# Kernel optimization log

Hardware: AMD Instinct MI355X
Metric: run time of the kernel (lower is better)

The kernel has to match this reference:

```python
import jax, jax.numpy as jnp
import numpy as np

B, S, D = 2, 2048, 1024
H = 16
HD = D // H
WINDOW = 128
SCALE = HD ** -0.5


def setup_inputs() -> dict:
    key = jax.random.key(0)
    ks = jax.random.split(key, 5)
    x = jax.random.normal(ks[0], (B, S, D), dtype=jnp.float32)
    # nn.Linear(dim, 3*dim) and nn.Linear(dim, dim), stored as [in, out] for x @ W
    w_qkv = jax.random.normal(ks[1], (D, 3 * D), dtype=jnp.float32) * (D ** -0.5)
    b_qkv = jax.random.normal(ks[2], (3 * D,), dtype=jnp.float32) * 0.02
    w_out = jax.random.normal(ks[3], (D, D), dtype=jnp.float32) * (D ** -0.5)
    b_out = jax.random.normal(ks[4], (D,), dtype=jnp.float32) * 0.02
    return {"x": x, "w_qkv": w_qkv, "b_qkv": b_qkv, "w_out": w_out, "b_out": b_out}


def _local_mask(seq_len):
    idx = jnp.arange(seq_len)
    band = jnp.abs(idx[:, None] - idx[None, :]) <= WINDOW // 2
    return jnp.where(band, 0.0, -jnp.inf).astype(jnp.float32)  # [S, S]


def reference(x, w_qkv, b_qkv, w_out, b_out):
    b, s, _ = x.shape
    qkv = x @ w_qkv + b_qkv                       # [B, S, 3D]
    qkv = qkv.reshape(b, s, 3, H, HD).transpose(2, 0, 3, 1, 4)  # [3, B, H, S, HD]
    q, k, v = qkv[0], qkv[1], qkv[2]
    mask = _local_mask(s)                          # [S, S]
    scores = jnp.einsum("bhqd,bhkd->bhqk", q, k) * SCALE + mask
    attn = jax.nn.softmax(scores, axis=-1)         # dropout is identity at eval
    out = jnp.einsum("bhqk,bhkd->bhqd", attn, v)   # [B, H, S, HD]
    out = out.transpose(0, 2, 1, 3).reshape(b, s, D)
    return out @ w_out + b_out
```

## Files before the change

### kernel.cpp

```cpp
#include <hip/hip_runtime.h>
#include <hip/hip_bf16.h>

typedef short bf16x8 __attribute__((ext_vector_type(8)));
typedef float f32x4 __attribute__((ext_vector_type(4)));
typedef unsigned short ushort_t;

#define SQ 2048
#define DIM 1024
#define NH 16
#define HD 64

__device__ __forceinline__ ushort_t f2bf(float f) {
    __hip_bfloat16 h = __float2bfloat16(f);
    return *reinterpret_cast<ushort_t*>(&h);
}

__device__ __forceinline__ void load_lds16(const void* g, void* l) {
    __builtin_amdgcn_global_load_lds(
        (const __attribute__((address_space(1))) unsigned int*)g,
        (__attribute__((address_space(3))) unsigned int*)l, 16, 0, 0);
}

__global__ void prep_kernel(const float* __restrict__ x, ushort_t* __restrict__ xb,
                            const float* __restrict__ w_qkv, ushort_t* __restrict__ wqkvT,
                            const float* __restrict__ w_out, ushort_t* __restrict__ woutT) {
    __shared__ ushort_t tile[32][33];
    const int bid = blockIdx.x;
    const int tid = threadIdx.x;
    if (bid < 1024) {
        int i = bid * 256 + tid;
        const int stride = 1024 * 256;
        const int n4 = 4096 * 1024 / 4;
        for (; i < n4; i += stride) {
            float4 f = reinterpret_cast<const float4*>(x)[i];
            ushort4 o;
            o.x = f2bf(f.x); o.y = f2bf(f.y); o.z = f2bf(f.z); o.w = f2bf(f.w);
            reinterpret_cast<ushort4*>(xb)[i] = o;
        }
        return;
    }
    const float* in; ushort_t* out; int R, C, idx;
    if (bid < 4096) { idx = bid - 1024; in = w_qkv; out = wqkvT; R = 1024; C = 3072;
        int cx = idx % 96, ry = idx / 96;
        int c0 = cx * 32, r0 = ry * 32;
        int tx = tid & 31, ty = tid >> 5;
#pragma unroll
        for (int i = 0; i < 32; i += 8)
            tile[ty + i][tx] = f2bf(in[(size_t)(r0 + ty + i) * C + c0 + tx]);
        __syncthreads();
#pragma unroll
        for (int i = 0; i < 32; i += 8)
            out[(size_t)(c0 + ty + i) * R + r0 + tx] = tile[tx][ty + i];
        return;
    }
    idx = bid - 4096; in = w_out; out = woutT; R = 1024; C = 1024;
    int cx = idx % 32, ry = idx / 32;
    int c0 = cx * 32, r0 = ry * 32;
    int tx = tid & 31, ty = tid >> 5;
#pragma unroll
    for (int i = 0; i < 32; i += 8)
        tile[ty + i][tx] = f2bf(in[(size_t)(r0 + ty + i) * C + c0 + tx]);
    __syncthreads();
#pragma unroll
    for (int i = 0; i < 32; i += 8)
        out[(size_t)(c0 + ty + i) * R + r0 + tx] = tile[tx][ty + i];
}

__global__ void transpose_v(const ushort_t* __restrict__ qkv, ushort_t* __restrict__ vt) {
    __shared__ ushort_t tile[32][33];
    int s0 = blockIdx.x * 32, d0 = blockIdx.y * 32;
    int bh = blockIdx.z;
    int b = bh >> 4, h = bh & 15;
    const ushort_t* src = qkv + (size_t)(b * SQ) * 3072 + 2048 + h * 64;
    ushort_t* dst = vt + (size_t)bh * HD * SQ;
    int tx = threadIdx.x, ty = threadIdx.y;
#pragma unroll
    for (int i = 0; i < 32; i += 8)
        tile[ty + i][tx] = src[(size_t)(s0 + ty + i) * 3072 + d0 + tx];
    __syncthreads();
#pragma unroll
    for (int i = 0; i < 32; i += 8)
        dst[(size_t)(d0 + ty + i) * SQ + s0 + tx] = tile[tx][ty + i];
}


#define STAGE_U(Gptr, ldk, grow0, kcol, regionbase)                          \
  { int row_ = tid >> 3;                                                      \
    int sc_ = (tid & 7) ^ (row_ & 7);                                         \
    load_lds16((Gptr) + (size_t)((grow0) + row_) * (ldk) + (kcol) + sc_ * 8,  \
               (regionbase) + tid * 16); }

#define DS_A192(BASE, EXTRA)                                                  \
  _Pragma("unroll") for (int kk_ = 0; kk_ < 2; ++kk_)                         \
  _Pragma("unroll") for (int m_ = 0; m_ < 4; ++m_)                            \
    a[kk_][m_] = *reinterpret_cast<const bf16x8*>((BASE) + (EXTRA) + offA[kk_][m_]);

#define DS_B192(BASE)                                                         \
  _Pragma("unroll") for (int kk_ = 0; kk_ < 2; ++kk_)                         \
  _Pragma("unroll") for (int n_ = 0; n_ < 3; ++n_)                            \
    b[kk_][n_] = *reinterpret_cast<const bf16x8*>((BASE) + offB[kk_][n_]);

#define BAR_LGKM                                                              \
  __builtin_amdgcn_s_barrier();                                               \
  asm volatile("s_waitcnt lgkmcnt(0)" ::: "memory");                          \
  __builtin_amdgcn_sched_barrier(0);

#define MFMA_Q(MQ)                                                            \
  __builtin_amdgcn_s_setprio(1);                                              \
  _Pragma("unroll") for (int kk_ = 0; kk_ < 2; ++kk_)                         \
  _Pragma("unroll") for (int m_ = 0; m_ < 4; ++m_)                            \
  _Pragma("unroll") for (int n_ = 0; n_ < 3; ++n_)                            \
    acc[(MQ)*4 + m_][n_] = __builtin_amdgcn_mfma_f32_16x16x32_bf16(           \
        a[kk_][m_], b[kk_][n_], acc[(MQ)*4 + m_][n_], 0, 0, 0);               \
  __builtin_amdgcn_s_setprio(0);

__global__ __launch_bounds__(512, 2)
void gemm192_bt(const ushort_t* __restrict__ A, const ushort_t* __restrict__ Bt,
                const float* __restrict__ bias, ushort_t* __restrict__ Cout,
                int M, int N, int K, int nbn) {
    __shared__ char sm[114688];
    const int tid = threadIdx.x;
    const int lane = tid & 63;
    const int w = tid >> 6;
    const int wm = w >> 2, wn = w & 3;
    const int r = lane & 15, hi = lane >> 4;

    const int cpx = gridDim.x >> 3;
    const int bid = blockIdx.x;
    const int x = (bid & 7) * cpx + (bid >> 3);
    const int bm = x / nbn, bn = x % nbn;
    const int m0 = bm * 256, n0 = bn * 192;

    const int NT = K >> 6;
    const int NI = NT >> 1;

    char* const A0 = sm;
    char* const B0 = sm + 32768;
    char* const A1 = sm + 57344;
    char* const B1 = sm + 90112;

    int offA[2][4], offB[2][3];
#pragma unroll
    for (int kk = 0; kk < 2; ++kk) {
#pragma unroll
        for (int m = 0; m < 4; ++m) {
            int rowL = wm * 128 + m * 16 + r;
            offA[kk][m] = rowL * 128 + (((kk * 4 + hi) ^ (rowL & 7)) * 16);
        }
#pragma unroll
        for (int n = 0; n < 3; ++n) {
            int rowL = wn * 48 + n * 16 + r;
            offB[kk][n] = rowL * 128 + (((kk * 4 + hi) ^ (rowL & 7)) * 16);
        }
    }

    f32x4 acc[8][3];
#pragma unroll
    for (int am = 0; am < 8; ++am)
#pragma unroll
        for (int an = 0; an < 3; ++an) acc[am][an] = (f32x4){0.f, 0.f, 0.f, 0.f};

    bf16x8 a[2][4], b[2][3];

    STAGE_U(A,  K, m0,        0, A0);
    STAGE_U(A,  K, m0 + 64,   0, A0 + 8192);
    STAGE_U(A,  K, m0 + 128,  0, A0 + 16384);
    STAGE_U(A,  K, m0 + 192,  0, A0 + 24576);
    STAGE_U(Bt, K, n0,        0, B0);
    STAGE_U(Bt, K, n0 + 64,   0, B0 + 8192);
    STAGE_U(Bt, K, n0 + 128,  0, B0 + 16384);
    STAGE_U(A,  K, m0,       64, A1);
    STAGE_U(A,  K, m0 + 128, 64, A1 + 16384);
    asm volatile("s_waitcnt vmcnt(2)" ::: "memory");
    __builtin_amdgcn_s_barrier();

    for (int i = 0; i < NI; ++i) {
        const int k1 = (2 * i + 1) * 64;
        const int k2 = ((2 * i + 2) % NT) * 64;
        const int k3 = ((2 * i + 3) % NT) * 64;

        STAGE_U(A,  K, m0 + 64,  k1, A1 + 8192);
        STAGE_U(A,  K, m0 + 192, k1, A1 + 24576);
        STAGE_U(Bt, K, n0,       k1, B1);
        STAGE_U(Bt, K, n0 + 64,  k1, B1 + 8192);
        STAGE_U(Bt, K, n0 + 128, k1, B1 + 16384);
        DS_A192(A0, 0); DS_B192(B0);
        BAR_LGKM; MFMA_Q(0);
        __builtin_amdgcn_s_barrier();

        STAGE_U(A, K, m0,       k2, A0);
        STAGE_U(A, K, m0 + 128, k2, A0 + 16384);
        DS_A192(A0, 8192);
        BAR_LGKM; MFMA_Q(1);
        asm volatile("s_waitcnt vmcnt(2)" ::: "memory");
        __builtin_amdgcn_s_barrier();

        STAGE_U(A,  K, m0 + 64,  k2, A0 + 8192);
        STAGE_U(A,  K, m0 + 192, k2, A0 + 24576);
        STAGE_U(Bt, K, n0,       k2, B0);
        STAGE_U(Bt, K, n0 + 64,  k2, B0 + 8192);
        STAGE_U(Bt, K, n0 + 128, k2, B0 + 16384);
        DS_A192(A1, 0); DS_B192(B1);
        BAR_LGKM; MFMA_Q(0);
        __builtin_amdgcn_s_barrier();

        STAGE_U(A, K, m0,       k3, A1);
        STAGE_U(A, K, m0 + 128, k3, A1 + 16384);
        DS_A192(A1, 8192);
        BAR_LGKM; MFMA_Q(1);
        asm volatile("s_waitcnt vmcnt(2)" ::: "memory");
        __builtin_amdgcn_s_barrier();
    }

#pragma unroll
    for (int am = 0; am < 8; ++am) {
        int rowg = m0 + wm * 128 + (am >> 2) * 64 + (am & 3) * 16 + hi * 4;
#pragma unroll
        for (int an = 0; an < 3; ++an) {
            int colg = n0 + wn * 48 + an * 16 + r;
            float bv = bias[colg];
#pragma unroll
            for (int j = 0; j < 4; ++j) {
                float v = acc[am][an][j] + bv;
                Cout[(size_t)(rowg + j) * N + colg] = f2bf(v);
            }
        }
    }
}

__global__ __launch_bounds__(256)
void gemm_bt2(const ushort_t* __restrict__ A, const ushort_t* __restrict__ Bt,
              const float* __restrict__ bias, float* __restrict__ Cout,
              int M, int N, int K) {
    __shared__ char sA[16384];
    __shared__ char sB[8192];
    const int tid = threadIdx.x;
    const int m0 = blockIdx.y * 128, n0 = blockIdx.x * 64;
    const int w = tid >> 6, lane = tid & 63;
    const int wr = w >> 1, wc = w & 1;
    const int r = lane & 15, hi = lane >> 4;

    f32x4 acc[4][2];
#pragma unroll
    for (int m = 0; m < 4; ++m)
#pragma unroll
        for (int n = 0; n < 2; ++n) acc[m][n] = (f32x4){0.f, 0.f, 0.f, 0.f};

    for (int k0 = 0; k0 < K; k0 += 64) {
#pragma unroll
        for (int i = 0; i < 4; ++i) {
            int task = i * 256 + tid;
            int row = task >> 3;
            int sc = (task & 7) ^ (row & 7);
            load_lds16(A + (size_t)(m0 + row) * K + k0 + sc * 8, sA + task * 16);
        }
#pragma unroll
        for (int i = 0; i < 2; ++i) {
            int task = i * 256 + tid;
            int row = task >> 3;
            int sc = (task & 7) ^ (row & 7);
            load_lds16(Bt + (size_t)(n0 + row) * K + k0 + sc * 8, sB + task * 16);
        }
        __syncthreads();

#pragma unroll
        for (int ks = 0; ks < 2; ++ks) {
            bf16x8 af[4], bfr[2];
#pragma unroll
            for (int m = 0; m < 4; ++m) {
                int row = wr * 64 + m * 16 + r;
                af[m] = *reinterpret_cast<const bf16x8*>(
                    sA + row * 128 + (((ks * 4 + hi) ^ (row & 7)) * 16));
            }
#pragma unroll
            for (int n = 0; n < 2; ++n) {
                int row = wc * 32 + n * 16 + r;
                bfr[n] = *reinterpret_cast<const bf16x8*>(
                    sB + row * 128 + (((ks * 4 + hi) ^ (row & 7)) * 16));
            }
#pragma unroll
            for (int m = 0; m < 4; ++m)
#pragma unroll
                for (int n = 0; n < 2; ++n)
                    acc[m][n] = __builtin_amdgcn_mfma_f32_16x16x32_bf16(
                        af[m], bfr[n], acc[m][n], 0, 0, 0);
        }
        __syncthreads();
    }

#pragma unroll
    for (int n = 0; n < 2; ++n) {
        int colg = n0 + wc * 32 + n * 16 + r;
        float bv = bias[colg];
#pragma unroll
        for (int m = 0; m < 4; ++m) {
            int rowg = m0 + wr * 64 + m * 16 + hi * 4;
#pragma unroll
            for (int j = 0; j < 4; ++j)
                Cout[(size_t)(rowg + j) * N + colg] = acc[m][n][j] + bv;
        }
    }
}

__global__ __launch_bounds__(256, 4)
void attn_kernel(const ushort_t* __restrict__ qkv, const ushort_t* __restrict__ vt,
                 ushort_t* __restrict__ attn_out) {
    __shared__ uint4 smem4[50176 / 16];
    char* smem = (char*)smem4;

    const int bid0 = blockIdx.x;
    const int bid = (bid0 & 7) * 128 + (bid0 >> 3);
    const int qb = bid & 31;
    const int h = (bid >> 5) & 15;
    const int b = bid >> 9;
    const int q0 = qb * 64;
    const int kstart = (q0 - 64 > 0) ? (q0 - 64) : 0;

    const int tid = threadIdx.x;
    const int lane = tid & 63;
    const int w = tid >> 6;
    const int r = lane & 15, hi = lane >> 4;

#pragma unroll
    for (int i = 0; i < 6; ++i) {
        int task = i * 256 + tid;
        int row = task >> 3, ch = task & 7;
        int key = kstart + row;
        uint4 v = make_uint4(0u, 0u, 0u, 0u);
        if (key < SQ)
            v = *reinterpret_cast<const uint4*>(
                qkv + (size_t)(b * SQ + key) * 3072 + 1024 + h * 64 + ch * 8);
        int byte = row * 128 + ch * 16; byte ^= (row & 7) << 4;
        *reinterpret_cast<uint4*>(smem + byte) = v;
    }
    {
        const ushort_t* vtb = vt + (size_t)(b * NH + h) * HD * SQ;
        int d = tid >> 2, cp = tid & 3;
#pragma unroll
        for (int i = 0; i < 6; ++i) {
            int c = cp + i * 4;
            uint4 v = make_uint4(0u, 0u, 0u, 0u);
            int k8 = kstart + c * 8;
            if (k8 < SQ)
                v = *reinterpret_cast<const uint4*>(vtb + (size_t)d * SQ + k8);
            int byte = d * 384 + (((c & 7) ^ (d & 7)) * 16) + ((c >> 3) * 128);
            *reinterpret_cast<uint4*>(smem + 25600 + byte) = v;
        }
    }

    const ushort_t* qrow = qkv + (size_t)(b * SQ + q0 + w * 16 + r) * 3072 + h * 64;
    bf16x8 aq0 = *reinterpret_cast<const bf16x8*>(qrow + hi * 8);
    bf16x8 aq1 = *reinterpret_cast<const bf16x8*>(qrow + 32 + hi * 8);

    __syncthreads();

    const int delta = q0 - kstart;
    const int base = w * 16 + delta;
    int tmin = (base - 64) >> 4; if (tmin < 0) tmin = 0;
    int tmax = (base + 79) >> 4;
    int tcap = (SQ - 1 - kstart) >> 4; if (tmax > tcap) tmax = tcap;
    if (tmax > 11) tmax = 11;
    const int ksmin = tmin >> 1, ksmax = tmax >> 1;

    f32x4 acc[12];
#pragma unroll
    for (int t = 0; t < 12; ++t) acc[t] = (f32x4){0.f, 0.f, 0.f, 0.f};
#pragma unroll
    for (int t = 0; t < 12; ++t) {
        if (t < tmin || t > tmax) continue;
#pragma unroll
        for (int ks = 0; ks < 2; ++ks) {
            int row = t * 16 + r;
            int byte = row * 128 + ks * 64 + hi * 16; byte ^= (row & 7) << 4;
            bf16x8 bk = *reinterpret_cast<const bf16x8*>(smem + byte);
            acc[t] = __builtin_amdgcn_mfma_f32_16x16x32_bf16(
                ks == 0 ? aq0 : aq1, bk, acc[t], 0, 0, 0);
        }
    }

    float mrow[4], lrow[4];
#pragma unroll
    for (int t = 0; t < 12; ++t) {
        if (t < tmin || t > tmax) continue;
        int key = kstart + t * 16 + r;
#pragma unroll
        for (int j = 0; j < 4; ++j) {
            int qrow_g = q0 + w * 16 + hi * 4 + j;
            int dd = key - qrow_g; if (dd < 0) dd = -dd;
            bool valid = (key < SQ) && (dd <= 64);
            acc[t][j] = valid ? acc[t][j] * 0.125f : -1e30f;
        }
    }
#pragma unroll
    for (int j = 0; j < 4; ++j) {
        float m = -1e30f;
#pragma unroll
        for (int t = 0; t < 12; ++t) {
            if (t < tmin || t > tmax) continue;
            m = fmaxf(m, acc[t][j]);
        }
        m = fmaxf(m, __shfl_xor(m, 1));
        m = fmaxf(m, __shfl_xor(m, 2));
        m = fmaxf(m, __shfl_xor(m, 4));
        m = fmaxf(m, __shfl_xor(m, 8));
        mrow[j] = m;
    }
#pragma unroll
    for (int j = 0; j < 4; ++j) {
        float s = 0.f;
#pragma unroll
        for (int t = 0; t < 12; ++t) {
            if (t < tmin || t > tmax) continue;
            float p = __expf(acc[t][j] - mrow[j]);
            acc[t][j] = p;
            s += p;
        }
        s += __shfl_xor(s, 1);
        s += __shfl_xor(s, 2);
        s += __shfl_xor(s, 4);
        s += __shfl_xor(s, 8);
        lrow[j] = s;
    }

    __syncthreads();

#pragma unroll
    for (int t = 0; t < 12; ++t) {
        int col = t * 16 + r;
        bool inb = (t >= tmin) && (t <= tmax);
#pragma unroll
        for (int j = 0; j < 4; ++j) {
            int rowL = w * 16 + hi * 4 + j;
            ushort_t pv = inb ? f2bf(acc[t][j]) : (ushort_t)0;
            *reinterpret_cast<ushort_t*>(smem + rowL * 400 + col * 2) = pv;
        }
    }

    f32x4 oacc[4];
#pragma unroll
    for (int dt = 0; dt < 4; ++dt) oacc[dt] = (f32x4){0.f, 0.f, 0.f, 0.f};
#pragma unroll
    for (int ks = 0; ks < 6; ++ks) {
        if (ks < ksmin || ks > ksmax) continue;
        int k0 = ks * 32 + hi * 8;
        bf16x8 ap = *reinterpret_cast<const bf16x8*>(
            smem + (w * 16 + r) * 400 + k0 * 2);
        int cch = ks * 4 + hi;
#pragma unroll
        for (int dt = 0; dt < 4; ++dt) {
            int d = dt * 16 + r;
            int byte = d * 384 + (((cch & 7) ^ (d & 7)) * 16) + ((cch >> 3) * 128);
            bf16x8 bv = *reinterpret_cast<const bf16x8*>(smem + 25600 + byte);
            oacc[dt] = __builtin_amdgcn_mfma_f32_16x16x32_bf16(ap, bv, oacc[dt], 0, 0, 0);
        }
    }

    float inv[4];
#pragma unroll
    for (int j = 0; j < 4; ++j) inv[j] = 1.0f / lrow[j];
#pragma unroll
    for (int dt = 0; dt < 4; ++dt) {
        int d = dt * 16 + r;
#pragma unroll
        for (int j = 0; j < 4; ++j) {
            int q = q0 + w * 16 + hi * 4 + j;
            attn_out[(size_t)(b * SQ + q) * 1024 + h * 64 + d] = f2bf(oacc[dt][j] * inv[j]);
        }
    }
}

extern "C" void kernel_launch(void* const* d_in, const int* in_sizes, int n_in,
                              void* d_out, int out_size, void* d_ws, size_t ws_size,
                              hipStream_t stream) {
    const float* x     = (const float*)d_in[0];
    const float* w_qkv = (const float*)d_in[1];
    const float* b_qkv = (const float*)d_in[2];
    const float* w_out = (const float*)d_in[3];
    const float* b_out = (const float*)d_in[4];
    float* out = (float*)d_out;

    char* ws = (char*)d_ws;
    ushort_t* xb    = (ushort_t*)(ws);
    ushort_t* wqkvT = (ushort_t*)(ws + 8388608);
    ushort_t* woutT = (ushort_t*)(ws + 14680064);
    ushort_t* qkv   = (ushort_t*)(ws + 16777216);
    ushort_t* aout  = (ushort_t*)(ws + 41943040);
    ushort_t* vtbuf = (ushort_t*)(ws + 50331648);

    prep_kernel<<<5120, 256, 0, stream>>>(x, xb, w_qkv, wqkvT, w_out, woutT);

    gemm192_bt<<<256, 512, 0, stream>>>(xb, wqkvT, b_qkv, qkv, 4096, 3072, 1024, 16);
    transpose_v<<<dim3(64, 2, 32), dim3(32, 8), 0, stream>>>(qkv, vtbuf);
    attn_kernel<<<1024, 256, 0, stream>>>(qkv, vtbuf, aout);
    gemm_bt2<<<dim3(16, 32), 256, 0, stream>>>(aout, woutT, b_out, out, 4096, 1024, 1024);
}
```

Before: 81.88 us.

## Replace output projection GEMM with double-buffered 128x128 four-phase pipelined kernel

The output projection GEMM, previously a 128x64 tile kernel that loads and then computes in single-buffered steps with two barriers per k-step, is replaced by a 512-thread 128x128 tile kernel. It double-buffers A and B in LDS and staggers global-to-LDS loads across four phases so loads overlap MFMA work, and it raises MFMA priority with s_setprio. Block IDs are swizzled across 8 groups. It reuses the STAGE_U and BAR_LGKM macros from the QKV GEMM. Grid size drops from 512 to 256 blocks, which may reduce occupancy on a 256-CU part.

```diff
diff --git a/kernel.cpp b/kernel.cpp
--- a/kernel.cpp
+++ b/kernel.cpp
@@ -228,76 +228,125 @@
     }
 }
 
-__global__ __launch_bounds__(256)
-void gemm_bt2(const ushort_t* __restrict__ A, const ushort_t* __restrict__ Bt,
-              const float* __restrict__ bias, float* __restrict__ Cout,
-              int M, int N, int K) {
-    __shared__ char sA[16384];
-    __shared__ char sB[8192];
+
+#define G2_DSA(BASE, MQ)                                                      \
+  _Pragma("unroll") for (int kk_ = 0; kk_ < 2; ++kk_)                         \
+  _Pragma("unroll") for (int m_ = 0; m_ < 2; ++m_)                            \
+    a2[kk_][m_] = *reinterpret_cast<const bf16x8*>((BASE) + offA2[kk_][(MQ)*2 + m_]);
+
+#define G2_DSB(BASE)                                                          \
+  _Pragma("unroll") for (int kk_ = 0; kk_ < 2; ++kk_)                         \
+  _Pragma("unroll") for (int n_ = 0; n_ < 2; ++n_)                            \
+    b2[kk_][n_] = *reinterpret_cast<const bf16x8*>((BASE) + offB2[kk_][n_]);
+
+#define G2_MFMA(MQ)                                                           \
+  __builtin_amdgcn_s_setprio(1);                                              \
+  _Pragma("unroll") for (int kk_ = 0; kk_ < 2; ++kk_)                         \
+  _Pragma("unroll") for (int m_ = 0; m_ < 2; ++m_)                            \
+  _Pragma("unroll") for (int n_ = 0; n_ < 2; ++n_)                            \
+    acc[(MQ)*2 + m_][n_] = __builtin_amdgcn_mfma_f32_16x16x32_bf16(           \
+        a2[kk_][m_], b2[kk_][n_], acc[(MQ)*2 + m_][n_], 0, 0, 0);             \
+  __builtin_amdgcn_s_setprio(0);
+
+__global__ __launch_bounds__(512, 2)
+void gemm128_4ph(const ushort_t* __restrict__ A, const ushort_t* __restrict__ Bt,
+                 const float* __restrict__ bias, float* __restrict__ Cout,
+                 int M, int N, int K, int nbn) {
+    __shared__ char sm[65536];
     const int tid = threadIdx.x;
-    const int m0 = blockIdx.y * 128, n0 = blockIdx.x * 64;
-    const int w = tid >> 6, lane = tid & 63;
-    const int wr = w >> 1, wc = w & 1;
+    const int lane = tid & 63;
+    const int w = tid >> 6;
+    const int wm = w >> 2, wn = w & 3;
     const int r = lane & 15, hi = lane >> 4;
 
+    const int cpx = gridDim.x >> 3;
+    const int bid = blockIdx.x;
+    const int x = (bid & 7) * cpx + (bid >> 3);
+    const int bm = x / nbn, bn = x % nbn;
+    const int m0 = bm * 128, n0 = bn * 128;
+
+    const int NT = K >> 6;
+    const int NI = NT >> 1;
+
+    char* const A0 = sm;
+    char* const B0 = sm + 16384;
+    char* const A1 = sm + 32768;
+    char* const B1 = sm + 49152;
+
+    int offA2[2][4], offB2[2][2];
+#pragma unroll
+    for (int kk = 0; kk < 2; ++kk) {
+#pragma unroll
+        for (int m = 0; m < 4; ++m) {
+            int rowL = wm * 64 + m * 16 + r;
+            offA2[kk][m] = rowL * 128 + (((kk * 4 + hi) ^ (rowL & 7)) * 16);
+        }
+#pragma unroll
+        for (int n = 0; n < 2; ++n) {
+            int rowL = wn * 32 + n * 16 + r;
+            offB2[kk][n] = rowL * 128 + (((kk * 4 + hi) ^ (rowL & 7)) * 16);
+        }
+    }
+
     f32x4 acc[4][2];
 #pragma unroll
-    for (int m = 0; m < 4; ++m)
-#pragma unroll
-        for (int n = 0; n < 2; ++n) acc[m][n] = (f32x4){0.f, 0.f, 0.f, 0.f};
-
-    for (int k0 = 0; k0 < K; k0 += 64) {
-#pragma unroll
-        for (int i = 0; i < 4; ++i) {
-            int task = i * 256 + tid;
-            int row = task >> 3;
-            int sc = (task & 7) ^ (row & 7);
-            load_lds16(A + (size_t)(m0 + row) * K + k0 + sc * 8, sA + task * 16);
-        }
-#pragma unroll
-        for (int i = 0; i < 2; ++i) {
-            int task = i * 256 + tid;
-            int row = task >> 3;
-            int sc = (task & 7) ^ (row & 7);
-            load_lds16(Bt + (size_t)(n0 + row) * K + k0 + sc * 8, sB + task * 16);
-        }
-        __syncthreads();
-
-#pragma unroll
-        for (int ks = 0; ks < 2; ++ks) {
-            bf16x8 af[4], bfr[2];
-#pragma unroll
-            for (int m = 0; m < 4; ++m) {
-                int row = wr * 64 + m * 16 + r;
-                af[m] = *reinterpret_cast<const bf16x8*>(
-                    sA + row * 128 + (((ks * 4 + hi) ^ (row & 7)) * 16));
-            }
-#pragma unroll
-            for (int n = 0; n < 2; ++n) {
-                int row = wc * 32 + n * 16 + r;
-                bfr[n] = *reinterpret_cast<const bf16x8*>(
-                    sB + row * 128 + (((ks * 4 + hi) ^ (row & 7)) * 16));
-            }
-#pragma unroll
-            for (int m = 0; m < 4; ++m)
-#pragma unroll
-                for (int n = 0; n < 2; ++n)
-                    acc[m][n] = __builtin_amdgcn_mfma_f32_16x16x32_bf16(
-                        af[m], bfr[n], acc[m][n], 0, 0, 0);
-        }
-        __syncthreads();
-    }
-
-#pragma unroll
-    for (int n = 0; n < 2; ++n) {
-        int colg = n0 + wc * 32 + n * 16 + r;
-        float bv = bias[colg];
-#pragma unroll
-        for (int m = 0; m < 4; ++m) {
-            int rowg = m0 + wr * 64 + m * 16 + hi * 4;
+    for (int am = 0; am < 4; ++am)
+#pragma unroll
+        for (int an = 0; an < 2; ++an) acc[am][an] = (f32x4){0.f, 0.f, 0.f, 0.f};
+
+    bf16x8 a2[2][2], b2[2][2];
+
+    STAGE_U(A,  K, m0,       0, A0);
+    STAGE_U(A,  K, m0 + 64,  0, A0 + 8192);
+    STAGE_U(Bt, K, n0,       0, B0);
+    STAGE_U(Bt, K, n0 + 64,  0, B0 + 8192);
+    STAGE_U(Bt, K, n0,      64, B1);
+    STAGE_U(Bt, K, n0 + 64, 64, B1 + 8192);
+    asm volatile("s_waitcnt vmcnt(2)" ::: "memory");
+    __builtin_amdgcn_s_barrier();
+
+    for (int i = 0; i < NI; ++i) {
+        const int k1 = (2 * i + 1) * 64;
+        const int k2 = ((2 * i + 2) % NT) * 64;
+        const int k3 = ((2 * i + 3) % NT) * 64;
+
+        STAGE_U(A, K, m0,      k1, A1);
+        STAGE_U(A, K, m0 + 64, k1, A1 + 8192);
+        G2_DSA(A0, 0); G2_DSB(B0);
+        BAR_LGKM; G2_MFMA(0);
+        __builtin_amdgcn_s_barrier();
+
+        STAGE_U(Bt, K, n0,      k2, B0);
+        STAGE_U(Bt, K, n0 + 64, k2, B0 + 8192);
+        G2_DSA(A0, 1);
+        BAR_LGKM; G2_MFMA(1);
+        asm volatile("s_waitcnt vmcnt(2)" ::: "memory");
+        __builtin_amdgcn_s_barrier();
+
+        STAGE_U(A, K, m0,      k2, A0);
+        STAGE_U(A, K, m0 + 64, k2, A0 + 8192);
+        G2_DSA(A1, 0); G2_DSB(B1);
+        BAR_LGKM; G2_MFMA(0);
+        __builtin_amdgcn_s_barrier();
+
+        STAGE_U(Bt, K, n0,      k3, B1);
+        STAGE_U(Bt, K, n0 + 64, k3, B1 + 8192);
+        G2_DSA(A1, 1);
+        BAR_LGKM; G2_MFMA(1);
+        asm volatile("s_waitcnt vmcnt(2)" ::: "memory");
+        __builtin_amdgcn_s_barrier();
+    }
+
+#pragma unroll
+    for (int am = 0; am < 4; ++am) {
+        int rowg = m0 + wm * 64 + am * 16 + hi * 4;
+#pragma unroll
+        for (int an = 0; an < 2; ++an) {
+            int colg = n0 + wn * 32 + an * 16 + r;
+            float bv = bias[colg];
 #pragma unroll
             for (int j = 0; j < 4; ++j)
-                Cout[(size_t)(rowg + j) * N + colg] = acc[m][n][j] + bv;
+                Cout[(size_t)(rowg + j) * N + colg] = acc[am][an][j] + bv;
         }
     }
 }
@@ -492,5 +541,5 @@
     gemm192_bt<<<256, 512, 0, stream>>>(xb, wqkvT, b_qkv, qkv, 4096, 3072, 1024, 16);
     transpose_v<<<dim3(64, 2, 32), dim3(32, 8), 0, stream>>>(qkv, vtbuf);
     attn_kernel<<<1024, 256, 0, stream>>>(qkv, vtbuf, aout);
-    gemm_bt2<<<dim3(16, 32), 256, 0, stream>>>(aout, woutT, b_out, out, 4096, 1024, 1024);
-}
+    gemm128_4ph<<<256, 512, 0, stream>>>(aout, woutT, b_out, out, 4096, 1024, 1024, 8);
+}
```

Result: faster. 78.42 us (-4.2%).
